# Kernel optimization log

Measured on AMD Instinct MI355X. Metric: run time of the kernel, lower is better.

Reference implementation:

```python
import jax, jax.numpy as jnp
import numpy as np

RADIUS = 5          # box-filter radius -> 11x11 kernel
TEMP = 0.5          # multinomial temperature
NSAMP = 5           # sampling_num
EPS = 1e-6
BN_EPS = 1e-5


def _conv(x, w, stride=1, padding=0, groups=1):
    return jax.lax.conv_general_dilated(
        x, w, window_strides=(stride, stride),
        padding=[(padding, padding), (padding, padding)],
        feature_group_count=groups,
        dimension_numbers=("NCHW", "OIHW", "NCHW"))


def custom_conv(x, w, key, stride=1, padding=0):
    """conv2d with cosine-activation regularization (bias=False path)."""
    B = x.shape[0]
    Cout = w.shape[0]
    # all-ones 'norm' conv on x*x
    x_norm = jnp.sqrt(_conv(x * x, jnp.ones_like(w), stride, padding))
    y = _conv(x, w, stride, padding)
    w_norm = jnp.sqrt(jnp.sum(w * w, axis=(1, 2, 3)))  # per-out-channel Frobenius norm
    cosine = y / (w_norm[None, :, None, None] + EPS) / (x_norm + EPS)
    # 11x11 depthwise box filter
    k = 2 * RADIUS + 1
    dw = jnp.ones((Cout, 1, k, k), x.dtype)
    cosine_mean = _conv(cosine, dw, 1, RADIUS, groups=Cout) / (k * k)
    H, W = cosine.shape[2], cosine.shape[3]
    # multinomial(NSAMP, exp(cosine/TEMP)) counts, no_grad in original
    logits = jax.lax.stop_gradient(cosine).reshape(B, Cout, H * W) / TEMP
    idx = jax.random.categorical(key, logits, axis=-1, shape=(NSAMP, B, Cout))
    bi = jnp.broadcast_to(jnp.arange(B)[None, :, None], (NSAMP, B, Cout))
    ci = jnp.broadcast_to(jnp.arange(Cout)[None, None, :], (NSAMP, B, Cout))
    mask = jnp.zeros((B, Cout, H * W), x.dtype).at[bi, ci, idx].add(1.0)
    cm = cosine_mean.reshape(B, Cout, H * W)
    act = ((mask * cm).sum(-1) / mask.sum(-1)).mean()
    return y, act


def batchnorm(x, g, b):
    # training-mode batch statistics (biased variance), like nn.BatchNorm2d
    m = x.mean(axis=(0, 2, 3), keepdims=True)
    v = x.var(axis=(0, 2, 3), keepdims=True)
    return (x - m) / jnp.sqrt(v + BN_EPS) * g[None, :, None, None] + b[None, :, None, None]


def setup_inputs() -> dict:
    key = jax.random.key(0)
    ks = jax.random.split(key, 10)
    x = jax.random.normal(ks[0], (16, 256, 56, 56), jnp.float32)
    w1 = jax.random.normal(ks[1], (64, 256, 1, 1), jnp.float32) * 0.05
    w2 = jax.random.normal(ks[2], (64, 64, 3, 3), jnp.float32) * 0.05
    w3 = jax.random.normal(ks[3], (256, 64, 1, 1), jnp.float32) * 0.05
    g1 = 1.0 + 0.05 * jax.random.normal(ks[4], (64,), jnp.float32)
    b1 = 0.05 * jax.random.normal(ks[5], (64,), jnp.float32)
    g2 = 1.0 + 0.05 * jax.random.normal(ks[6], (64,), jnp.float32)
    b2 = 0.05 * jax.random.normal(ks[7], (64,), jnp.float32)
    g3 = 1.0 + 0.05 * jax.random.normal(ks[8], (256,), jnp.float32)
    b3 = 0.05 * jax.random.normal(ks[9], (256,), jnp.float32)
    return {"x": x, "w1": w1, "w2": w2, "w3": w3,
            "g1": g1, "b1": b1, "g2": g2, "b2": b2, "g3": g3, "b3": b3}


def reference(x, w1, w2, w3, g1, b1, g2, b2, g3, b3):
    k0, k1, k2 = jax.random.split(jax.random.key(42), 3)
    acc = jnp.asarray(0.0, x.dtype)
    out, a = custom_conv(x, w1, k0)           # conv1x1
    acc = acc + a
    out = jax.nn.relu(batchnorm(out, g1, b1))
    out, a = custom_conv(out, w2, k1, padding=1)  # conv3x3, stride 1
    acc = acc + a
    out = jax.nn.relu(batchnorm(out, g2, b2))
    out, a = custom_conv(out, w3, k2)         # conv1x1 expand
    acc = acc + a
    out = batchnorm(out, g3, b3)
    out = jax.nn.relu(out + x)                # identity shortcut (downsample=None)
    return out, acc
```

## Files before the change

kernel.cpp:

```cpp
#include <hip/hip_runtime.h>
#include <stdint.h>
#include <math.h>

#define HW 3136
#define NPIX 50176

typedef __attribute__((ext_vector_type(8))) short bf16x8;
typedef __attribute__((ext_vector_type(4))) float f32x4;
#define MFMA16(a, b, c) __builtin_amdgcn_mfma_f32_16x16x32_bf16(a, b, c, 0, 0, 0)

__device__ __forceinline__ unsigned short f2bf(float f) {
  unsigned u = __float_as_uint(f);
  u = (u + 0x7fffu + ((u >> 16) & 1u)) >> 16;
  return (unsigned short)u;
}
__device__ __forceinline__ unsigned pk2(float a, float b) {
  return (unsigned)f2bf(a) | ((unsigned)f2bf(b) << 16);
}
__device__ __forceinline__ float bf2f(unsigned short h) {
  return __uint_as_float(((unsigned)h) << 16);
}

__host__ __device__ __forceinline__ uint32_t rotl32(uint32_t v, int r) {
  return (v << r) | (v >> (32 - r));
}

__host__ __device__ inline void threefry2x32(uint32_t k0, uint32_t k1,
                                             uint32_t x0, uint32_t x1,
                                             uint32_t& o0, uint32_t& o1) {
  uint32_t k2 = k0 ^ k1 ^ 0x1BD11BDAu;
  x0 += k0; x1 += k1;
  x0 += x1; x1 = rotl32(x1, 13); x1 ^= x0;
  x0 += x1; x1 = rotl32(x1, 15); x1 ^= x0;
  x0 += x1; x1 = rotl32(x1, 26); x1 ^= x0;
  x0 += x1; x1 = rotl32(x1, 6);  x1 ^= x0;
  x0 += k1; x1 += k2 + 1u;
  x0 += x1; x1 = rotl32(x1, 17); x1 ^= x0;
  x0 += x1; x1 = rotl32(x1, 29); x1 ^= x0;
  x0 += x1; x1 = rotl32(x1, 16); x1 ^= x0;
  x0 += x1; x1 = rotl32(x1, 24); x1 ^= x0;
  x0 += k2; x1 += k0 + 2u;
  x0 += x1; x1 = rotl32(x1, 13); x1 ^= x0;
  x0 += x1; x1 = rotl32(x1, 15); x1 ^= x0;
  x0 += x1; x1 = rotl32(x1, 26); x1 ^= x0;
  x0 += x1; x1 = rotl32(x1, 6);  x1 ^= x0;
  x0 += k0; x1 += k1 + 3u;
  x0 += x1; x1 = rotl32(x1, 17); x1 ^= x0;
  x0 += x1; x1 = rotl32(x1, 29); x1 ^= x0;
  x0 += x1; x1 = rotl32(x1, 16); x1 ^= x0;
  x0 += x1; x1 = rotl32(x1, 24); x1 ^= x0;
  x0 += k1; x1 += k2 + 4u;
  x0 += x1; x1 = rotl32(x1, 13); x1 ^= x0;
  x0 += x1; x1 = rotl32(x1, 15); x1 ^= x0;
  x0 += x1; x1 = rotl32(x1, 26); x1 ^= x0;
  x0 += x1; x1 = rotl32(x1, 6);  x1 ^= x0;
  x0 += k2; x1 += k0 + 5u;
  o0 = x0; o1 = x1;
}

#define TF5_R(r)                                            \
  _Pragma("unroll") for (int i = 0; i < 5; ++i) {           \
    x0[i] += x1[i]; x1[i] = rotl32(x1[i], r) ^ x0[i];       \
  }
#define TF5_INJ(a, b)                                       \
  _Pragma("unroll") for (int i = 0; i < 5; ++i) {           \
    x0[i] += (a); x1[i] += (b);                             \
  }
__device__ __forceinline__ void threefry5(uint32_t k0, uint32_t k1,
    const uint32_t xa[5], const uint32_t xb[5], uint32_t oa[5], uint32_t ob[5]) {
  uint32_t k2 = k0 ^ k1 ^ 0x1BD11BDAu;
  uint32_t x0[5], x1[5];
  #pragma unroll
  for (int i = 0; i < 5; ++i) { x0[i] = xa[i] + k0; x1[i] = xb[i] + k1; }
  TF5_R(13) TF5_R(15) TF5_R(26) TF5_R(6)  TF5_INJ(k1, k2 + 1u)
  TF5_R(17) TF5_R(29) TF5_R(16) TF5_R(24) TF5_INJ(k2, k0 + 2u)
  TF5_R(13) TF5_R(15) TF5_R(26) TF5_R(6)  TF5_INJ(k0, k1 + 3u)
  TF5_R(17) TF5_R(29) TF5_R(16) TF5_R(24) TF5_INJ(k1, k2 + 4u)
  TF5_R(13) TF5_R(15) TF5_R(26) TF5_R(6)  TF5_INJ(k2, k0 + 5u)
  #pragma unroll
  for (int i = 0; i < 5; ++i) { oa[i] = x0[i]; ob[i] = x1[i]; }
}

#define LN2F 0.6931471805599453f
__device__ __forceinline__ float gumbel_from_bits(uint32_t bits) {
  float u = __uint_as_float((bits >> 9) | 0x3f800000u) - 1.0f;
  u = fmaxf(u, 1.17549435e-38f);
  float t = __log2f(u);
  float inner = LN2F * (-t);
  return -LN2F * __log2f(inner);
}

__global__ void wprep_k(const float* __restrict__ w1, const float* __restrict__ w2,
                        const float* __restrict__ w3, float* __restrict__ invwn,
                        unsigned short* __restrict__ W1b, unsigned short* __restrict__ W2tb,
                        unsigned short* __restrict__ W3b) {
  int i = blockIdx.x * 256 + threadIdx.x;
  if (i < 16384) {
    W1b[i] = f2bf(w1[i]);
  } else if (i < 53248) {
    int o = i - 16384;
    int co = o / 576, r = o % 576, tap = r >> 6, ci = r & 63;
    W2tb[o] = f2bf(w2[co * 576 + ci * 9 + tap]);
  } else if (i < 69632) {
    int o = i - 53248;
    W3b[o] = f2bf(w3[o]);
  } else {
    int t = i - 69632;
    if (t < 64) {
      float s = 0.f;
      for (int k = 0; k < 256; k++) { float v = w1[t * 256 + k]; s = fmaf(v, v, s); }
      invwn[t] = 1.0f / (sqrtf(s) + 1e-6f);
    } else if (t < 128) {
      int c = t - 64; float s = 0.f;
      for (int k = 0; k < 576; k++) { float v = w2[c * 576 + k]; s = fmaf(v, v, s); }
      invwn[t] = 1.0f / (sqrtf(s) + 1e-6f);
    } else if (t < 384) {
      int c = t - 128; float s = 0.f;
      for (int k = 0; k < 64; k++) { float v = w3[c * 64 + k]; s = fmaf(v, v, s); }
      invwn[t] = 1.0f / (sqrtf(s) + 1e-6f);
    }
  }
}

__global__ __launch_bounds__(256) void bn_fin(const float* __restrict__ Sp,
    const float* __restrict__ Qp, const float* __restrict__ g,
    const float* __restrict__ b, float* __restrict__ sc, float* __restrict__ sh,
    int nblk) {
  const int c = blockIdx.x, tid = threadIdx.x;
  const float* rs = Sp + (size_t)c * nblk;
  const float* rq = Qp + (size_t)c * nblk;
  float s = 0.f, q = 0.f;
  for (int i = tid; i < nblk; i += 256) { s += rs[i]; q += rq[i]; }
  #pragma unroll
  for (int o = 32; o; o >>= 1) { s += __shfl_xor(s, o); q += __shfl_xor(q, o); }
  __shared__ float S[4], Q[4];
  int lane = tid & 63, wave = tid >> 6;
  if (lane == 0) { S[wave] = s; Q[wave] = q; }
  __syncthreads();
  if (tid == 0) {
    float st = S[0] + S[1] + S[2] + S[3];
    float qt = Q[0] + Q[1] + Q[2] + Q[3];
    float mean = st * (1.0f / (float)NPIX);
    float var = qt * (1.0f / (float)NPIX) - mean * mean;
    float sv = g[c] / sqrtf(var + 1e-5f);
    sc[c] = sv; sh[c] = b[c] - mean * sv;
  }
}

__global__ __launch_bounds__(256) void conv1_mfma(
    const float* __restrict__ X, const unsigned short* __restrict__ Wb,
    const float* __restrict__ invwn, unsigned short* __restrict__ Y1,
    unsigned short* __restrict__ CS, float* __restrict__ Sp, float* __restrict__ Qp) {
#define ST1 264
#define NB1 784
  __shared__ __align__(16) unsigned short bq[64 * ST1];
  __shared__ float sqp[4][64];
  __shared__ float ixn[64];
  const int p0 = blockIdx.x * 64, b = blockIdx.y;
  const int bid = b * 49 + blockIdx.x;
  const int tid = threadIdx.x;
  const int lane = tid & 63, wave = tid >> 6;
  const int m = lane & 15, quad = lane >> 4;
  const int co0 = wave * 16;
  const float* Xb = X + (size_t)b * 256 * HW + p0;

  bf16x8 afr[8];
  const unsigned short* wrow = Wb + (co0 + m) * 256 + quad * 8;
  #pragma unroll
  for (int k = 0; k < 8; ++k) afr[k] = *(const bf16x8*)(wrow + k * 32);

  {
    const int px = tid & 63, rg = tid >> 6;
    float sq = 0.f;
    #pragma unroll
    for (int it = 0; it < 16; ++it) {
      int ci = rg * 64 + it * 4;
      float v0 = Xb[(size_t)(ci + 0) * HW + px];
      float v1 = Xb[(size_t)(ci + 1) * HW + px];
      float v2 = Xb[(size_t)(ci + 2) * HW + px];
      float v3 = Xb[(size_t)(ci + 3) * HW + px];
      sq += v0 * v0 + v1 * v1 + v2 * v2 + v3 * v3;
      *(uint2*)&bq[px * ST1 + ci] = make_uint2(pk2(v0, v1), pk2(v2, v3));
    }
    sqp[rg][px] = sq;
  }
  __syncthreads();
  if (tid < 64)
    ixn[tid] = 1.0f / (sqrtf(sqp[0][tid] + sqp[1][tid] + sqp[2][tid] + sqp[3][tid]) + 1e-6f);
  __syncthreads();

  f32x4 acc[4];
  #pragma unroll
  for (int nt = 0; nt < 4; ++nt) acc[nt] = (f32x4)0.f;
  #pragma unroll
  for (int nt = 0; nt < 4; ++nt) {
    const unsigned short* brow = &bq[(nt * 16 + m) * ST1 + quad * 8];
    #pragma unroll
    for (int k = 0; k < 8; ++k) {
      bf16x8 bfrag = *(const bf16x8*)(brow + k * 32);
      acc[nt] = MFMA16(afr[k], bfrag, acc[nt]);
    }
  }

  float s[4] = {0, 0, 0, 0}, q[4] = {0, 0, 0, 0};
  #pragma unroll
  for (int nt = 0; nt < 4; ++nt) {
    int px = nt * 16 + m;
    size_t bp = (size_t)b * HW + p0 + px;
    float ix = ixn[px];
    *(uint2*)&Y1[bp * 64 + co0 + quad * 4] =
        make_uint2(pk2(acc[nt][0], acc[nt][1]), pk2(acc[nt][2], acc[nt][3]));
    #pragma unroll
    for (int r = 0; r < 4; ++r) {
      int co = co0 + quad * 4 + r;
      float v = acc[nt][r];
      CS[((size_t)b * 64 + co) * HW + p0 + px] = f2bf(v * invwn[co] * ix);
      s[r] += v; q[r] = fmaf(v, v, q[r]);
    }
  }
  #pragma unroll
  for (int r = 0; r < 4; ++r) {
    float ss = s[r], qq = q[r];
    #pragma unroll
    for (int o = 8; o; o >>= 1) { ss += __shfl_xor(ss, o); qq += __shfl_xor(qq, o); }
    if (m == 0) {
      int co = co0 + quad * 4 + r;
      Sp[(size_t)co * NB1 + bid] = ss; Qp[(size_t)co * NB1 + bid] = qq;
    }
  }
#undef NB1
#undef ST1
}

__global__ __launch_bounds__(256) void chansum_px(const unsigned short* __restrict__ Y1,
    const float* __restrict__ sc, const float* __restrict__ sh,
    float* __restrict__ part) {
  int g = blockIdx.x * 256 + threadIdx.x;
  const unsigned short* row = Y1 + (size_t)g * 64;
  float s = 0.f;
  #pragma unroll
  for (int j = 0; j < 8; ++j) {
    uint4 d = *(const uint4*)(row + j * 8);
    unsigned dd[4] = {d.x, d.y, d.z, d.w};
    #pragma unroll
    for (int e = 0; e < 4; ++e) {
      int c = j * 8 + e * 2;
      float v0 = fmaxf(0.f, fmaf(bf2f((unsigned short)(dd[e] & 0xffff)), sc[c], sh[c]));
      float v1 = fmaxf(0.f, fmaf(bf2f((unsigned short)(dd[e] >> 16)), sc[c + 1], sh[c + 1]));
      s = fmaf(v0, v0, s); s = fmaf(v1, v1, s);
    }
  }
  part[g] = s;
}

__global__ __launch_bounds__(256) void box3inv(const float* __restrict__ part,
                                               float* __restrict__ out) {
  int g = blockIdx.x * 256 + threadIdx.x;
  int b = g / HW, p = g - b * HW;
  int y = p / 56, x = p % 56;
  float tot = 0.f;
  for (int dy = -1; dy <= 1; dy++) {
    int yy = y + dy; if (yy < 0 || yy >= 56) continue;
    for (int dx = -1; dx <= 1; dx++) {
      int xx = x + dx; if (xx < 0 || xx >= 56) continue;
      tot += part[b * HW + yy * 56 + xx];
    }
  }
  out[g] = 1.0f / (sqrtf(tot) + 1e-6f);
}

__global__ __launch_bounds__(256) void conv2_mfma(
    const unsigned short* __restrict__ Y1, const unsigned short* __restrict__ W2tb,
    const float* __restrict__ invwn, const float* __restrict__ ixn2,
    const float* __restrict__ sc1, const float* __restrict__ sh1,
    unsigned short* __restrict__ Y2, unsigned short* __restrict__ CS,
    float* __restrict__ Sp, float* __restrict__ Qp) {
#define STW 72
#define NB2 896
  __shared__ __align__(16) unsigned short ts[3 * 66 * STW];
  __shared__ float scl[64], shl[64];
  const int h = blockIdx.x, b = blockIdx.y;
  const int bid = b * 56 + h;
  const int tid = threadIdx.x;
  const int lane = tid & 63, wave = tid >> 6;
  const int m = lane & 15, quad = lane >> 4;
  const int co0 = wave * 16;
  if (tid < 64) { scl[tid] = sc1[tid]; shl[tid] = sh1[tid]; }

  bf16x8 afr[18];
  #pragma unroll
  for (int ks = 0; ks < 18; ++ks)
    afr[ks] = *(const bf16x8*)(W2tb + (co0 + m) * 576 + ks * 32 + quad * 8);
  __syncthreads();

  for (int l = tid; l < 6336; l += 256) {
    int cp = l & 31, cc = (l >> 5) % 66, dy = l / 2112;
    int yy = h - 1 + dy, xx = cc - 1;
    unsigned pkv = 0u;
    if (yy >= 0 && yy < 56 && xx >= 0 && xx < 56) {
      unsigned d = *(const unsigned*)&Y1[((size_t)b * HW + yy * 56 + xx) * 64 + cp * 2];
      float v0 = bf2f((unsigned short)(d & 0xffff));
      float v1 = bf2f((unsigned short)(d >> 16));
      v0 = fmaxf(0.f, fmaf(v0, scl[cp * 2], shl[cp * 2]));
      v1 = fmaxf(0.f, fmaf(v1, scl[cp * 2 + 1], shl[cp * 2 + 1]));
      pkv = pk2(v0, v1);
    }
    *(unsigned*)&ts[(dy * 66 + cc) * STW + cp * 2] = pkv;
  }
  __syncthreads();

  f32x4 acc[4];
  #pragma unroll
  for (int nt = 0; nt < 4; ++nt) acc[nt] = (f32x4)0.f;
  #pragma unroll
  for (int nt = 0; nt < 4; ++nt) {
    #pragma unroll
    for (int ks = 0; ks < 18; ++ks) {
      int tap = ks >> 1, half = ks & 1;
      int dy = tap / 3, dx = tap % 3;
      bf16x8 bfrag = *(const bf16x8*)&ts[(dy * 66 + nt * 16 + m + dx) * STW + half * 32 + quad * 8];
      acc[nt] = MFMA16(afr[ks], bfrag, acc[nt]);
    }
  }

  float s[4] = {0, 0, 0, 0}, q[4] = {0, 0, 0, 0};
  #pragma unroll
  for (int nt = 0; nt < 4; ++nt) {
    int px = nt * 16 + m;
    bool valid = px < 56;
    int pix = h * 56 + px;
    if (valid) {
      float ix = ixn2[b * HW + pix];
      size_t bp = (size_t)b * HW + pix;
      *(uint2*)&Y2[bp * 64 + co0 + quad * 4] =
          make_uint2(pk2(acc[nt][0], acc[nt][1]), pk2(acc[nt][2], acc[nt][3]));
      #pragma unroll
      for (int r = 0; r < 4; ++r) {
        int co = co0 + quad * 4 + r;
        CS[((size_t)b * 64 + co) * HW + pix] = f2bf(acc[nt][r] * invwn[co] * ix);
      }
    }
    #pragma unroll
    for (int r = 0; r < 4; ++r) {
      float v = valid ? acc[nt][r] : 0.f;
      s[r] += v; q[r] = fmaf(v, v, q[r]);
    }
  }
  #pragma unroll
  for (int r = 0; r < 4; ++r) {
    float ss = s[r], qq = q[r];
    #pragma unroll
    for (int o = 8; o; o >>= 1) { ss += __shfl_xor(ss, o); qq += __shfl_xor(qq, o); }
    if (m == 0) {
      int co = co0 + quad * 4 + r;
      Sp[(size_t)co * NB2 + bid] = ss; Qp[(size_t)co * NB2 + bid] = qq;
    }
  }
#undef NB2
#undef STW
}

__global__ __launch_bounds__(256) void conv3_mfma(
    const unsigned short* __restrict__ Y2, const unsigned short* __restrict__ W3b,
    const float* __restrict__ invwn,
    const float* __restrict__ sc2, const float* __restrict__ sh2,
    unsigned short* __restrict__ Y3, unsigned short* __restrict__ CS,
    float* __restrict__ Sp, float* __restrict__ Qp) {
#define ST3 72
#define NB3 784
  __shared__ __align__(16) unsigned short bq[64 * ST3];
  __shared__ float scl[64], shl[64], sqp[4][64], ixn[64];
  const int p0 = blockIdx.x * 64, b = blockIdx.y;
  const int bid = b * 49 + blockIdx.x;
  const int tid = threadIdx.x;
  const int lane = tid & 63, wave = tid >> 6;
  const int m = lane & 15, quad = lane >> 4;
  const int co0 = wave * 64;
  if (tid < 64) { scl[tid] = sc2[tid]; shl[tid] = sh2[tid]; }

  bf16x8 afr[4][2];
  #pragma unroll
  for (int mt = 0; mt < 4; ++mt)
    #pragma unroll
    for (int k = 0; k < 2; ++k)
      afr[mt][k] = *(const bf16x8*)(W3b + (co0 + mt * 16 + m) * 64 + k * 32 + quad * 8);
  __syncthreads();

  {
    const int cp = tid & 31, pxg = tid >> 5;
    #pragma unroll
    for (int it = 0; it < 8; ++it) {
      int px = pxg * 8 + it;
      unsigned d = *(const unsigned*)&Y2[((size_t)b * HW + p0 + px) * 64 + cp * 2];
      float v0 = bf2f((unsigned short)(d & 0xffff));
      float v1 = bf2f((unsigned short)(d >> 16));
      v0 = fmaxf(0.f, fmaf(v0, scl[cp * 2], shl[cp * 2]));
      v1 = fmaxf(0.f, fmaf(v1, scl[cp * 2 + 1], shl[cp * 2 + 1]));
      *(unsigned*)&bq[px * ST3 + cp * 2] = pk2(v0, v1);
    }
  }
  __syncthreads();
  {
    const int px = tid & 63, hh = tid >> 6;
    const unsigned short* row = &bq[px * ST3 + hh * 16];
    float sq = 0.f;
    #pragma unroll
    for (int e = 0; e < 16; ++e) { float v = bf2f(row[e]); sq = fmaf(v, v, sq); }
    sqp[hh][px] = sq;
  }
  __syncthreads();
  if (tid < 64)
    ixn[tid] = 1.0f / (sqrtf(sqp[0][tid] + sqp[1][tid] + sqp[2][tid] + sqp[3][tid]) + 1e-6f);
  __syncthreads();

  f32x4 acc[4][4];
  #pragma unroll
  for (int mt = 0; mt < 4; ++mt)
    #pragma unroll
    for (int nt = 0; nt < 4; ++nt) acc[mt][nt] = (f32x4)0.f;
  #pragma unroll
  for (int nt = 0; nt < 4; ++nt) {
    const unsigned short* brow = &bq[(nt * 16 + m) * ST3 + quad * 8];
    bf16x8 b0 = *(const bf16x8*)(brow);
    bf16x8 b1 = *(const bf16x8*)(brow + 32);
    #pragma unroll
    for (int mt = 0; mt < 4; ++mt) {
      acc[mt][nt] = MFMA16(afr[mt][0], b0, acc[mt][nt]);
      acc[mt][nt] = MFMA16(afr[mt][1], b1, acc[mt][nt]);
    }
  }

  #pragma unroll
  for (int mt = 0; mt < 4; ++mt) {
    float s[4] = {0, 0, 0, 0}, q[4] = {0, 0, 0, 0};
    #pragma unroll
    for (int nt = 0; nt < 4; ++nt) {
      int px = nt * 16 + m;
      float ix = ixn[px];
      #pragma unroll
      for (int r = 0; r < 4; ++r) {
        int co = co0 + mt * 16 + quad * 4 + r;
        float v = acc[mt][nt][r];
        size_t off = ((size_t)b * 256 + co) * HW + p0 + px;
        Y3[off] = f2bf(v);
        CS[off] = f2bf(v * invwn[co] * ix);
        s[r] += v; q[r] = fmaf(v, v, q[r]);
      }
    }
    #pragma unroll
    for (int r = 0; r < 4; ++r) {
      float ss = s[r], qq = q[r];
      #pragma unroll
      for (int o = 8; o; o >>= 1) { ss += __shfl_xor(ss, o); qq += __shfl_xor(qq, o); }
      if (m == 0) {
        int co = co0 + mt * 16 + quad * 4 + r;
        Sp[(size_t)co * NB3 + bid] = ss; Qp[(size_t)co * NB3 + bid] = qq;
      }
    }
  }
#undef NB3
#undef ST3
}

__global__ __launch_bounds__(256, 4) void sample5_k(const unsigned short* __restrict__ CS,
    float* __restrict__ acc, uint32_t key0, uint32_t key1, int BC, float scale) {
  const int u = blockIdx.x;
  const int v = u + (BC >> 1);
  const uint32_t sC = (uint32_t)BC * (uint32_t)HW;
  const uint32_t halfn = sC * 2u + (sC >> 1);
  const unsigned short* rowU = CS + (size_t)u * HW;
  const unsigned short* rowV = CS + (size_t)v * HW;
  const int tid = threadIdx.x;
  const int lane = tid & 63, wave = tid >> 6;

  float bst[10]; int idx[10];
  #pragma unroll
  for (int k = 0; k < 10; ++k) { bst[k] = -INFINITY; idx[k] = 0; }

  const uint32_t baseU0 = (uint32_t)u * (uint32_t)HW;
  const uint32_t baseV0 = (uint32_t)v * (uint32_t)HW;
  for (int p = tid; p < HW; p += 256) {
    float lu = 2.0f * bf2f(rowU[p]);
    float lv = 2.0f * bf2f(rowV[p]);
    uint32_t eU = baseU0 + (uint32_t)p;
    uint32_t eV = baseV0 + (uint32_t)p;
    uint32_t xa[5] = {eU, eU + sC, eU + 2 * sC, eV, eV + sC};
    uint32_t xb[5] = {eU + halfn, eU + sC + halfn, eU + 2 * sC + halfn,
                      eV + halfn, eV + sC + halfn};
    uint32_t oa[5], ob[5];
    threefry5(key0, key1, xa, xb, oa, ob);
    float gu[5], gv[5];
    gu[0] = gumbel_from_bits(oa[0]);
    gu[1] = gumbel_from_bits(oa[1]);
    gu[2] = gumbel_from_bits(oa[2]);
    gu[3] = gumbel_from_bits(ob[3]);
    gu[4] = gumbel_from_bits(ob[4]);
    gv[0] = gumbel_from_bits(oa[3]);
    gv[1] = gumbel_from_bits(oa[4]);
    gv[2] = gumbel_from_bits(ob[0]);
    gv[3] = gumbel_from_bits(ob[1]);
    gv[4] = gumbel_from_bits(ob[2]);
    #pragma unroll
    for (int k = 0; k < 5; ++k) {
      float su = lu + gu[k];
      float sv = lv + gv[k];
      if (su > bst[k])     { bst[k] = su;     idx[k] = p; }
      if (sv > bst[5 + k]) { bst[5 + k] = sv; idx[5 + k] = p; }
    }
  }

  __shared__ float rv[10][4];
  __shared__ int   ri[10][4];
  __shared__ int   widx[10];
  __shared__ float wsum[10];
  #pragma unroll
  for (int k = 0; k < 10; ++k) {
    float val = bst[k]; int ix = idx[k];
    #pragma unroll
    for (int o = 32; o; o >>= 1) {
      float ov = __shfl_xor(val, o); int oi = __shfl_xor(ix, o);
      if (ov > val || (ov == val && oi < ix)) { val = ov; ix = oi; }
    }
    if (lane == 0) { rv[k][wave] = val; ri[k][wave] = ix; }
  }
  if (tid < 10) wsum[tid] = 0.f;
  __syncthreads();
  if (tid < 10) {
    float val = rv[tid][0]; int ix = ri[tid][0];
    #pragma unroll
    for (int wv = 1; wv < 4; ++wv) {
      float ov = rv[tid][wv]; int oi = ri[tid][wv];
      if (ov > val || (ov == val && oi < ix)) { val = ov; ix = oi; }
    }
    widx[tid] = ix;
  }
  __syncthreads();

  int c2 = tid >> 7, j = tid & 127;
  if (j < 121) {
    int dy = j / 11 - 5, dxx = j % 11 - 5;
    #pragma unroll
    for (int k = 0; k < 5; ++k) {
      int win = k * 2 + c2;
      int bidx = widx[win];
      int py = bidx / 56, px = bidx % 56;
      int yy = py + dy, xx = px + dxx;
      if (yy >= 0 && yy < 56 && xx >= 0 && xx < 56) {
        const unsigned short* row = (win < 5) ? rowU : rowV;
        atomicAdd(&wsum[win], bf2f(row[yy * 56 + xx]));
      }
    }
  }
  __syncthreads();
  if (tid == 0) {
    float t = 0.f;
    #pragma unroll
    for (int k = 0; k < 10; ++k) t += wsum[k];
    atomicAdd(acc, t * scale);
  }
}

__global__ __launch_bounds__(256) void final_k(const unsigned short* __restrict__ Y3,
    const float* __restrict__ X, const float* __restrict__ sc,
    const float* __restrict__ sh, const float* __restrict__ acc,
    float* __restrict__ out) {
  size_t i4 = (size_t)blockIdx.x * 256 + threadIdx.x;
  if (i4 == 0) out[12845056] = acc[0];
  size_t i = i4 * 4;
  int c = (int)((i / HW) % 256);
  float a = sc[c], d = sh[c];
  uint2 yd = *(const uint2*)&Y3[i];
  float4 xv = *(const float4*)&X[i];
  float4 r;
  r.x = fmaxf(0.f, fmaf(bf2f((unsigned short)(yd.x & 0xffff)), a, d) + xv.x);
  r.y = fmaxf(0.f, fmaf(bf2f((unsigned short)(yd.x >> 16)),    a, d) + xv.y);
  r.z = fmaxf(0.f, fmaf(bf2f((unsigned short)(yd.y & 0xffff)), a, d) + xv.z);
  r.w = fmaxf(0.f, fmaf(bf2f((unsigned short)(yd.y >> 16)),    a, d) + xv.w);
  *(float4*)&out[i] = r;
}

extern "C" void kernel_launch(void* const* d_in, const int* in_sizes, int n_in,
                              void* d_out, int out_size, void* d_ws, size_t ws_size,
                              hipStream_t stream) {
  (void)in_sizes; (void)n_in; (void)out_size; (void)ws_size;
  const float* x  = (const float*)d_in[0];
  const float* w1 = (const float*)d_in[1];
  const float* w2 = (const float*)d_in[2];
  const float* w3 = (const float*)d_in[3];
  const float* g1 = (const float*)d_in[4];
  const float* b1 = (const float*)d_in[5];
  const float* g2 = (const float*)d_in[6];
  const float* b2 = (const float*)d_in[7];
  const float* g3 = (const float*)d_in[8];
  const float* b3 = (const float*)d_in[9];
  float* out = (float*)d_out;
  float* ws = (float*)d_ws;

  size_t o = 0;
  unsigned short* y3b  = (unsigned short*)(ws + o); o += 6422528;
  unsigned short* cos3 = (unsigned short*)(ws + o); o += 6422528;
  unsigned short* CSb  = (unsigned short*)(ws + o); o += 1605632;
  unsigned short* y1b  = (unsigned short*)(ws + o); o += 1605632;
  unsigned short* y2b  = (unsigned short*)(ws + o); o += 1605632;
  unsigned short* W1b  = (unsigned short*)(ws + o); o += 8192;
  unsigned short* W2tb = (unsigned short*)(ws + o); o += 18432;
  unsigned short* W3b  = (unsigned short*)(ws + o); o += 8192;
  float* part = ws + o; o += NPIX;
  float* ixn2 = ws + o; o += NPIX;
  float* invwn = ws + o; o += 384;
  float* Sp1 = ws + o; o += 64 * 784;   float* Qp1 = ws + o; o += 64 * 784;
  float* Sp2 = ws + o; o += 64 * 896;   float* Qp2 = ws + o; o += 64 * 896;
  float* Sp3 = ws + o; o += 256 * 784;  float* Qp3 = ws + o; o += 256 * 784;
  float* acc = ws + o; o += 1;
  float* sc1 = ws + o; o += 64;  float* sh1 = ws + o; o += 64;
  float* sc2 = ws + o; o += 64;  float* sh2 = ws + o; o += 64;
  float* sc3 = ws + o; o += 256; float* sh3 = ws + o; o += 256;

  hipMemsetAsync(acc, 0, sizeof(float), stream);

  uint32_t A0, B0, A1, B1, A2, B2;
  threefry2x32(0u, 42u, 0u, 3u, A0, B0);
  threefry2x32(0u, 42u, 1u, 4u, A1, B1);
  threefry2x32(0u, 42u, 2u, 5u, A2, B2);

  const float scale64  = 1.0f / (121.0f * 5.0f * 1024.0f);
  const float scale256 = 1.0f / (121.0f * 5.0f * 4096.0f);

  wprep_k<<<274, 256, 0, stream>>>(w1, w2, w3, invwn, W1b, W2tb, W3b);

  conv1_mfma<<<dim3(49, 16), 256, 0, stream>>>(x, W1b, invwn, y1b, CSb, Sp1, Qp1);
  bn_fin<<<64, 256, 0, stream>>>(Sp1, Qp1, g1, b1, sc1, sh1, 784);
  sample5_k<<<512, 256, 0, stream>>>(CSb, acc, A0, A1, 1024, scale64);

  chansum_px<<<196, 256, 0, stream>>>(y1b, sc1, sh1, part);
  box3inv<<<196, 256, 0, stream>>>(part, ixn2);
  conv2_mfma<<<dim3(56, 16), 256, 0, stream>>>(
      y1b, W2tb, invwn + 64, ixn2, sc1, sh1, y2b, CSb, Sp2, Qp2);
  bn_fin<<<64, 256, 0, stream>>>(Sp2, Qp2, g2, b2, sc2, sh2, 896);
  sample5_k<<<512, 256, 0, stream>>>(CSb, acc, A2, B0, 1024, scale64);

  conv3_mfma<<<dim3(49, 16), 256, 0, stream>>>(
      y2b, W3b, invwn + 128, sc2, sh2, y3b, cos3, Sp3, Qp3);
  bn_fin<<<256, 256, 0, stream>>>(Sp3, Qp3, g3, b3, sc3, sh3, 784);
  sample5_k<<<2048, 256, 0, stream>>>(cos3, acc, B1, B2, 4096, scale256);
  final_k<<<12544, 256, 0, stream>>>(y3b, x, sc3, sh3, acc, out);
}
```

Baseline: 400.7 us.

## Replace Gumbel-max sampling with exponential-race argmin using packed integer keys

The sampler swaps the Gumbel-max argmax, which needs two logs per draw, for an equivalent exponential race: it draws E = -ln(u), scales it by exp(-2·logit) and takes the argmin. This needs one log per draw plus one exp2 per pixel. The float score and the pixel index are packed into one 32-bit key by masking low mantissa bits, so the reductions become plain integer mins with a shared atomicMin. Block size becomes a template parameter, with 512 threads for the 64-channel layers and a flattened box-sum loop. Truncating the mantissa can break near-ties differently from the reference, which slightly changes which pixels are sampled.

```diff
diff --git a/kernel.cpp b/kernel.cpp
--- a/kernel.cpp
+++ b/kernel.cpp
@@ -21,46 +21,44 @@
   return __uint_as_float(((unsigned)h) << 16);
 }
 
-__host__ __device__ __forceinline__ uint32_t rotl32(uint32_t v, int r) {
-  return (v << r) | (v >> (32 - r));
-}
+#define ROTL32(v, r) __builtin_rotateleft32((uint32_t)(v), (r))
 
 __host__ __device__ inline void threefry2x32(uint32_t k0, uint32_t k1,
                                              uint32_t x0, uint32_t x1,
                                              uint32_t& o0, uint32_t& o1) {
   uint32_t k2 = k0 ^ k1 ^ 0x1BD11BDAu;
   x0 += k0; x1 += k1;
-  x0 += x1; x1 = rotl32(x1, 13); x1 ^= x0;
-  x0 += x1; x1 = rotl32(x1, 15); x1 ^= x0;
-  x0 += x1; x1 = rotl32(x1, 26); x1 ^= x0;
-  x0 += x1; x1 = rotl32(x1, 6);  x1 ^= x0;
+  x0 += x1; x1 = ROTL32(x1, 13); x1 ^= x0;
+  x0 += x1; x1 = ROTL32(x1, 15); x1 ^= x0;
+  x0 += x1; x1 = ROTL32(x1, 26); x1 ^= x0;
+  x0 += x1; x1 = ROTL32(x1, 6);  x1 ^= x0;
   x0 += k1; x1 += k2 + 1u;
-  x0 += x1; x1 = rotl32(x1, 17); x1 ^= x0;
-  x0 += x1; x1 = rotl32(x1, 29); x1 ^= x0;
-  x0 += x1; x1 = rotl32(x1, 16); x1 ^= x0;
-  x0 += x1; x1 = rotl32(x1, 24); x1 ^= x0;
+  x0 += x1; x1 = ROTL32(x1, 17); x1 ^= x0;
+  x0 += x1; x1 = ROTL32(x1, 29); x1 ^= x0;
+  x0 += x1; x1 = ROTL32(x1, 16); x1 ^= x0;
+  x0 += x1; x1 = ROTL32(x1, 24); x1 ^= x0;
   x0 += k2; x1 += k0 + 2u;
-  x0 += x1; x1 = rotl32(x1, 13); x1 ^= x0;
-  x0 += x1; x1 = rotl32(x1, 15); x1 ^= x0;
-  x0 += x1; x1 = rotl32(x1, 26); x1 ^= x0;
-  x0 += x1; x1 = rotl32(x1, 6);  x1 ^= x0;
+  x0 += x1; x1 = ROTL32(x1, 13); x1 ^= x0;
+  x0 += x1; x1 = ROTL32(x1, 15); x1 ^= x0;
+  x0 += x1; x1 = ROTL32(x1, 26); x1 ^= x0;
+  x0 += x1; x1 = ROTL32(x1, 6);  x1 ^= x0;
   x0 += k0; x1 += k1 + 3u;
-  x0 += x1; x1 = rotl32(x1, 17); x1 ^= x0;
-  x0 += x1; x1 = rotl32(x1, 29); x1 ^= x0;
-  x0 += x1; x1 = rotl32(x1, 16); x1 ^= x0;
-  x0 += x1; x1 = rotl32(x1, 24); x1 ^= x0;
+  x0 += x1; x1 = ROTL32(x1, 17); x1 ^= x0;
+  x0 += x1; x1 = ROTL32(x1, 29); x1 ^= x0;
+  x0 += x1; x1 = ROTL32(x1, 16); x1 ^= x0;
+  x0 += x1; x1 = ROTL32(x1, 24); x1 ^= x0;
   x0 += k1; x1 += k2 + 4u;
-  x0 += x1; x1 = rotl32(x1, 13); x1 ^= x0;
-  x0 += x1; x1 = rotl32(x1, 15); x1 ^= x0;
-  x0 += x1; x1 = rotl32(x1, 26); x1 ^= x0;
-  x0 += x1; x1 = rotl32(x1, 6);  x1 ^= x0;
+  x0 += x1; x1 = ROTL32(x1, 13); x1 ^= x0;
+  x0 += x1; x1 = ROTL32(x1, 15); x1 ^= x0;
+  x0 += x1; x1 = ROTL32(x1, 26); x1 ^= x0;
+  x0 += x1; x1 = ROTL32(x1, 6);  x1 ^= x0;
   x0 += k2; x1 += k0 + 5u;
   o0 = x0; o1 = x1;
 }
 
 #define TF5_R(r)                                            \
   _Pragma("unroll") for (int i = 0; i < 5; ++i) {           \
-    x0[i] += x1[i]; x1[i] = rotl32(x1[i], r) ^ x0[i];       \
+    x0[i] += x1[i]; x1[i] = ROTL32(x1[i], r) ^ x0[i];       \
   }
 #define TF5_INJ(a, b)                                       \
   _Pragma("unroll") for (int i = 0; i < 5; ++i) {           \
@@ -81,13 +79,12 @@
   for (int i = 0; i < 5; ++i) { oa[i] = x0[i]; ob[i] = x1[i]; }
 }
 
-#define LN2F 0.6931471805599453f
-__device__ __forceinline__ float gumbel_from_bits(uint32_t bits) {
+#define NLN2F -0.6931471805599453f
+#define NEG2LOG2E -2.8853900817779268f
+__device__ __forceinline__ float exp_draw(uint32_t bits) {
   float u = __uint_as_float((bits >> 9) | 0x3f800000u) - 1.0f;
   u = fmaxf(u, 1.17549435e-38f);
-  float t = __log2f(u);
-  float inner = LN2F * (-t);
-  return -LN2F * __log2f(inner);
+  return NLN2F * __log2f(u);
 }
 
 __global__ void wprep_k(const float* __restrict__ w1, const float* __restrict__ w2,
@@ -462,7 +459,8 @@
 #undef ST3
 }
 
-__global__ __launch_bounds__(256, 4) void sample5_k(const unsigned short* __restrict__ CS,
+template <int NT>
+__global__ __launch_bounds__(NT) void sample5_k(const unsigned short* __restrict__ CS,
     float* __restrict__ acc, uint32_t key0, uint32_t key1, int BC, float scale) {
   const int u = blockIdx.x;
   const int v = u + (BC >> 1);
@@ -471,17 +469,21 @@
   const unsigned short* rowU = CS + (size_t)u * HW;
   const unsigned short* rowV = CS + (size_t)v * HW;
   const int tid = threadIdx.x;
-  const int lane = tid & 63, wave = tid >> 6;
-
-  float bst[10]; int idx[10];
-  #pragma unroll
-  for (int k = 0; k < 10; ++k) { bst[k] = -INFINITY; idx[k] = 0; }
+  const int lane = tid & 63;
+
+  __shared__ unsigned kmin[10];
+  __shared__ float wsum[10];
+  if (tid < 10) { kmin[tid] = 0xFFFFFFFFu; wsum[tid] = 0.f; }
+
+  unsigned bk[10];
+  #pragma unroll
+  for (int k = 0; k < 10; ++k) bk[k] = 0xFFFFFFFFu;
 
   const uint32_t baseU0 = (uint32_t)u * (uint32_t)HW;
   const uint32_t baseV0 = (uint32_t)v * (uint32_t)HW;
-  for (int p = tid; p < HW; p += 256) {
-    float lu = 2.0f * bf2f(rowU[p]);
-    float lv = 2.0f * bf2f(rowV[p]);
+  for (int p = tid; p < HW; p += NT) {
+    float wu = __builtin_amdgcn_exp2f(bf2f(rowU[p]) * NEG2LOG2E);
+    float wv = __builtin_amdgcn_exp2f(bf2f(rowV[p]) * NEG2LOG2E);
     uint32_t eU = baseU0 + (uint32_t)p;
     uint32_t eV = baseV0 + (uint32_t)p;
     uint32_t xa[5] = {eU, eU + sC, eU + 2 * sC, eV, eV + sC};
@@ -489,66 +491,37 @@
                       eV + halfn, eV + sC + halfn};
     uint32_t oa[5], ob[5];
     threefry5(key0, key1, xa, xb, oa, ob);
-    float gu[5], gv[5];
-    gu[0] = gumbel_from_bits(oa[0]);
-    gu[1] = gumbel_from_bits(oa[1]);
-    gu[2] = gumbel_from_bits(oa[2]);
-    gu[3] = gumbel_from_bits(ob[3]);
-    gu[4] = gumbel_from_bits(ob[4]);
-    gv[0] = gumbel_from_bits(oa[3]);
-    gv[1] = gumbel_from_bits(oa[4]);
-    gv[2] = gumbel_from_bits(ob[0]);
-    gv[3] = gumbel_from_bits(ob[1]);
-    gv[4] = gumbel_from_bits(ob[2]);
-    #pragma unroll
-    for (int k = 0; k < 5; ++k) {
-      float su = lu + gu[k];
-      float sv = lv + gv[k];
-      if (su > bst[k])     { bst[k] = su;     idx[k] = p; }
-      if (sv > bst[5 + k]) { bst[5 + k] = sv; idx[5 + k] = p; }
-    }
-  }
-
-  __shared__ float rv[10][4];
-  __shared__ int   ri[10][4];
-  __shared__ int   widx[10];
-  __shared__ float wsum[10];
+    uint32_t wds[10] = {oa[0], oa[1], oa[2], ob[3], ob[4],
+                        oa[3], oa[4], ob[0], ob[1], ob[2]};
+    #pragma unroll
+    for (int k = 0; k < 10; ++k) {
+      float s = exp_draw(wds[k]) * (k < 5 ? wu : wv);
+      unsigned key = (__float_as_uint(s) & 0xFFFFF000u) | (unsigned)p;
+      bk[k] = bk[k] < key ? bk[k] : key;
+    }
+  }
+
+  __syncthreads();
   #pragma unroll
   for (int k = 0; k < 10; ++k) {
-    float val = bst[k]; int ix = idx[k];
+    unsigned kv = bk[k];
     #pragma unroll
     for (int o = 32; o; o >>= 1) {
-      float ov = __shfl_xor(val, o); int oi = __shfl_xor(ix, o);
-      if (ov > val || (ov == val && oi < ix)) { val = ov; ix = oi; }
-    }
-    if (lane == 0) { rv[k][wave] = val; ri[k][wave] = ix; }
-  }
-  if (tid < 10) wsum[tid] = 0.f;
-  __syncthreads();
-  if (tid < 10) {
-    float val = rv[tid][0]; int ix = ri[tid][0];
-    #pragma unroll
-    for (int wv = 1; wv < 4; ++wv) {
-      float ov = rv[tid][wv]; int oi = ri[tid][wv];
-      if (ov > val || (ov == val && oi < ix)) { val = ov; ix = oi; }
-    }
-    widx[tid] = ix;
-  }
-  __syncthreads();
-
-  int c2 = tid >> 7, j = tid & 127;
-  if (j < 121) {
-    int dy = j / 11 - 5, dxx = j % 11 - 5;
-    #pragma unroll
-    for (int k = 0; k < 5; ++k) {
-      int win = k * 2 + c2;
-      int bidx = widx[win];
-      int py = bidx / 56, px = bidx % 56;
-      int yy = py + dy, xx = px + dxx;
-      if (yy >= 0 && yy < 56 && xx >= 0 && xx < 56) {
-        const unsigned short* row = (win < 5) ? rowU : rowV;
-        atomicAdd(&wsum[win], bf2f(row[yy * 56 + xx]));
-      }
+      unsigned ov = __shfl_xor(kv, o);
+      kv = kv < ov ? kv : ov;
+    }
+    if (lane == 0) atomicMin(&kmin[k], kv);
+  }
+  __syncthreads();
+
+  for (int idx = tid; idx < 1210; idx += NT) {
+    int win = idx / 121, j = idx - win * 121;
+    int bidx = (int)(kmin[win] & 0xFFFu);
+    int py = bidx / 56, px = bidx % 56;
+    int yy = py + j / 11 - 5, xx = px + j % 11 - 5;
+    if (yy >= 0 && yy < 56 && xx >= 0 && xx < 56) {
+      const unsigned short* row = (win < 5) ? rowU : rowV;
+      atomicAdd(&wsum[win], bf2f(row[yy * 56 + xx]));
     }
   }
   __syncthreads();
@@ -630,18 +603,18 @@
 
   conv1_mfma<<<dim3(49, 16), 256, 0, stream>>>(x, W1b, invwn, y1b, CSb, Sp1, Qp1);
   bn_fin<<<64, 256, 0, stream>>>(Sp1, Qp1, g1, b1, sc1, sh1, 784);
-  sample5_k<<<512, 256, 0, stream>>>(CSb, acc, A0, A1, 1024, scale64);
+  sample5_k<512><<<512, 512, 0, stream>>>(CSb, acc, A0, A1, 1024, scale64);
 
   chansum_px<<<196, 256, 0, stream>>>(y1b, sc1, sh1, part);
   box3inv<<<196, 256, 0, stream>>>(part, ixn2);
   conv2_mfma<<<dim3(56, 16), 256, 0, stream>>>(
       y1b, W2tb, invwn + 64, ixn2, sc1, sh1, y2b, CSb, Sp2, Qp2);
   bn_fin<<<64, 256, 0, stream>>>(Sp2, Qp2, g2, b2, sc2, sh2, 896);
-  sample5_k<<<512, 256, 0, stream>>>(CSb, acc, A2, B0, 1024, scale64);
+  sample5_k<512><<<512, 512, 0, stream>>>(CSb, acc, A2, B0, 1024, scale64);
 
   conv3_mfma<<<dim3(49, 16), 256, 0, stream>>>(
       y2b, W3b, invwn + 128, sc2, sh2, y3b, cos3, Sp3, Qp3);
   bn_fin<<<256, 256, 0, stream>>>(Sp3, Qp3, g3, b3, sc3, sh3, 784);
-  sample5_k<<<2048, 256, 0, stream>>>(cos3, acc, B1, B2, 4096, scale256);
+  sample5_k<256><<<2048, 256, 0, stream>>>(cos3, acc, B1, B2, 4096, scale256);
   final_k<<<12544, 256, 0, stream>>>(y3b, x, sc3, sh3, acc, out);
 }
```

Result: faster. 382.3 us (-4.6%).
